# Kernel optimization log

Hardware: AMD Instinct MI355X
Metric: run time of the kernel (lower is better)

The kernel has to match this reference:

```python
import jax, jax.numpy as jnp
import numpy as np

N_NODES = 100000
N_EDGES = 3200000
F_IN = 128
F_OUT = 128


def setup_inputs() -> dict:
    key = jax.random.key(0)
    ks = jax.random.split(key, 6)
    stdv = 1.0 / np.sqrt(F_OUT)
    return {
        "x": jax.random.normal(ks[0], (N_NODES, F_IN), dtype=jnp.float32),
        "weight": jax.random.uniform(ks[1], (F_IN, F_OUT), minval=-stdv, maxval=stdv, dtype=jnp.float32),
        "bias": jax.random.uniform(ks[2], (F_OUT,), minval=-stdv, maxval=stdv, dtype=jnp.float32),
        "edge_src": jax.random.randint(ks[3], (N_EDGES,), 0, N_NODES, dtype=jnp.int32),
        "edge_dst": jax.random.randint(ks[4], (N_EDGES,), 0, N_NODES, dtype=jnp.int32),
        "edge_weight": jax.random.uniform(ks[5], (N_EDGES,), dtype=jnp.float32),
    }


def reference(x, weight, bias, edge_src, edge_dst, edge_weight):
    # Dense feature transform: support = X @ W  -> [N, F_OUT]
    support = jnp.matmul(x, weight)
    # Sparse adjacency aggregation (SpMM): out[d] = sum_e A[d, s_e] * support[s_e]
    msgs = support[edge_src] * edge_weight[:, None]  # [E, F_OUT]
    out = jax.ops.segment_sum(msgs, edge_dst, num_segments=N_NODES)
    return out + bias
```

## Files before the change

### kernel.cpp

```cpp
#include <hip/hip_runtime.h>

#define F 128
#define NB 64
#define MAXB 2048
#define NCHUNK 512
#define BCAP 3072

typedef __bf16 bf16x8 __attribute__((ext_vector_type(8)));
typedef unsigned short u16x8 __attribute__((ext_vector_type(8)));
typedef float f32x4 __attribute__((ext_vector_type(4)));

static __device__ __forceinline__ unsigned short f2bf(float f) {
    unsigned u = __float_as_uint(f);
    unsigned r = (u + 0x7FFF + ((u >> 16) & 1)) >> 16;
    return (unsigned short)r;
}

static __device__ __forceinline__ unsigned pack_rec(int src, int dl, float w) {
    unsigned wfix = (unsigned)(w * 511.0f + 0.5f);
    if (wfix > 511u) wfix = 511u;
    return (unsigned)src | ((unsigned)dl << 17) | (wfix << 23);
}

__global__ __launch_bounds__(256) void gemm_hist_kernel(const float* __restrict__ X,
                                                        const float* __restrict__ W,
                                                        unsigned short* __restrict__ Sb,
                                                        int n_nodes,
                                                        const int* __restrict__ edst,
                                                        int* __restrict__ counts,
                                                        int* __restrict__ bcnt,
                                                        int n_edges, int nbuck, int epc,
                                                        int ngemm) {
    __shared__ char smem[F * F * 2];
    int t = threadIdx.x;

    if ((int)blockIdx.x < ngemm) {
        unsigned short* WT = (unsigned short*)smem;
        {
            int f = t >> 1, half = t & 1;
#pragma unroll
            for (int j = 0; j < 8; ++j) {
                int k0 = half * 64 + j * 8;
                u16x8 pk;
#pragma unroll
                for (int i = 0; i < 8; ++i) pk[i] = f2bf(W[(size_t)(k0 + i) * F + f]);
                int byte = f * 256 + ((k0 * 2) ^ ((f & 7) << 4));
                *(u16x8*)((char*)WT + byte) = pk;
            }
        }
        __syncthreads();

        int w = t >> 6, l = t & 63;
        int lr = l & 15, lg = l >> 4;
        int rowBase = blockIdx.x * 128 + w * 32;

        f32x4 acc[2][8] = {};
        int r0 = rowBase + lr;
        int r1 = rowBase + 16 + lr;
        if (r0 >= n_nodes) r0 = n_nodes - 1;
        if (r1 >= n_nodes) r1 = n_nodes - 1;
        const float* a0p = X + (size_t)r0 * F + lg * 8;
        const float* a1p = X + (size_t)r1 * F + lg * 8;

#pragma unroll
        for (int kt = 0; kt < 4; ++kt) {
            float4 x0 = *(const float4*)(a0p + kt * 32);
            float4 x1 = *(const float4*)(a0p + kt * 32 + 4);
            u16x8 au;
            au[0] = f2bf(x0.x); au[1] = f2bf(x0.y); au[2] = f2bf(x0.z); au[3] = f2bf(x0.w);
            au[4] = f2bf(x1.x); au[5] = f2bf(x1.y); au[6] = f2bf(x1.z); au[7] = f2bf(x1.w);
            bf16x8 a0 = __builtin_bit_cast(bf16x8, au);
            float4 y0 = *(const float4*)(a1p + kt * 32);
            float4 y1 = *(const float4*)(a1p + kt * 32 + 4);
            au[0] = f2bf(y0.x); au[1] = f2bf(y0.y); au[2] = f2bf(y0.z); au[3] = f2bf(y0.w);
            au[4] = f2bf(y1.x); au[5] = f2bf(y1.y); au[6] = f2bf(y1.z); au[7] = f2bf(y1.w);
            bf16x8 a1 = __builtin_bit_cast(bf16x8, au);
#pragma unroll
            for (int ct = 0; ct < 8; ++ct) {
                int f = ct * 16 + lr;
                int byte = f * 256 + (((kt * 32 + lg * 8) * 2) ^ ((f & 7) << 4));
                bf16x8 bfr = *(bf16x8*)((char*)WT + byte);
                acc[0][ct] = __builtin_amdgcn_mfma_f32_16x16x32_bf16(a0, bfr, acc[0][ct], 0, 0, 0);
                acc[1][ct] = __builtin_amdgcn_mfma_f32_16x16x32_bf16(a1, bfr, acc[1][ct], 0, 0, 0);
            }
        }

#pragma unroll
        for (int tile = 0; tile < 2; ++tile) {
#pragma unroll
            for (int ct = 0; ct < 8; ++ct) {
                int col = ct * 16 + lr;
#pragma unroll
                for (int j = 0; j < 4; ++j) {
                    int row = rowBase + tile * 16 + lg * 4 + j;
                    if (row < n_nodes) Sb[(size_t)row * F + col] = f2bf(acc[tile][ct][j]);
                }
            }
        }
    } else {
        int* h = (int*)smem;
        int c = blockIdx.x - ngemm;
        for (int i = t; i < nbuck; i += 256) h[i] = 0;
        __syncthreads();
        int beg = c * epc, end = min(n_edges, beg + epc);
        for (int e0 = beg + t * 4; e0 < end; e0 += 1024) {
            if (e0 + 4 <= end) {
                int4 d4 = *(const int4*)&edst[e0];
                atomicAdd(&h[d4.x >> 6], 1);
                atomicAdd(&h[d4.y >> 6], 1);
                atomicAdd(&h[d4.z >> 6], 1);
                atomicAdd(&h[d4.w >> 6], 1);
            } else {
                for (int e = e0; e < end; ++e) atomicAdd(&h[edst[e] >> 6], 1);
            }
        }
        __syncthreads();
        for (int i = t; i < nbuck; i += 256) {
            int v = h[i];
            counts[(size_t)c * nbuck + i] = v;
            if (v) __hip_atomic_fetch_add(&bcnt[i], v, __ATOMIC_RELAXED, __HIP_MEMORY_SCOPE_AGENT);
        }
    }
}

__global__ __launch_bounds__(256) void bscan_kernel(const int* __restrict__ bcnt,
                                                    int* __restrict__ bstart, int nbuck) {
    __shared__ int tsum[256];
    int t = threadIdx.x;
    const int EPT = MAXB / 256;
    int base = t * EPT;
    int v[EPT];
    int s = 0;
#pragma unroll
    for (int i = 0; i < EPT; ++i) {
        int idx = base + i;
        v[i] = (idx < nbuck) ? bcnt[idx] : 0;
        s += v[i];
    }
    tsum[t] = s;
    __syncthreads();
    for (int off = 1; off < 256; off <<= 1) {
        int x = (t >= off) ? tsum[t - off] : 0;
        __syncthreads();
        tsum[t] += x;
        __syncthreads();
    }
    int run = tsum[t] - s;
#pragma unroll
    for (int i = 0; i < EPT; ++i) {
        int idx = base + i;
        if (idx < nbuck) {
            bstart[idx] = run;
            run += v[i];
        }
    }
    if (t == 255) bstart[nbuck] = run;
}

__global__ __launch_bounds__(256) void chunk_offs_kernel(const int* __restrict__ counts,
                                                         const int* __restrict__ bstart,
                                                         int* __restrict__ offs, int nbuck) {
    int wv = threadIdx.x >> 6, l = threadIdx.x & 63;
    int b = blockIdx.x * 4 + wv;
    if (b >= nbuck) return;
    const int CPL = NCHUNK / 64;
    int base = l * CPL;
    int v[CPL];
    int s = 0;
#pragma unroll
    for (int i = 0; i < CPL; ++i) {
        v[i] = counts[(size_t)(base + i) * nbuck + b];
        s += v[i];
    }
    int inc = s;
#pragma unroll
    for (int off = 1; off < 64; off <<= 1) {
        int up = __shfl_up(inc, off, 64);
        if (l >= off) inc += up;
    }
    int run = bstart[b] + inc - s;
#pragma unroll
    for (int i = 0; i < CPL; ++i) {
        offs[(size_t)(base + i) * nbuck + b] = run;
        run += v[i];
    }
}

__global__ __launch_bounds__(256) void chunk_scatter_kernel(const int* __restrict__ esrc,
                                                            const int* __restrict__ edst,
                                                            const float* __restrict__ ew,
                                                            const int* __restrict__ offs,
                                                            unsigned* __restrict__ ebuf,
                                                            int n_edges, int nbuck, int epc) {
    __shared__ int lcur[MAXB];
    int c = blockIdx.x, t = threadIdx.x;
    for (int i = t; i < nbuck; i += 256) lcur[i] = offs[(size_t)c * nbuck + i];
    __syncthreads();
    int beg = c * epc, end = min(n_edges, beg + epc);
    for (int e0 = beg + t * 4; e0 < end; e0 += 1024) {
        if (e0 + 4 <= end) {
            int4 s4 = *(const int4*)&esrc[e0];
            int4 d4 = *(const int4*)&edst[e0];
            float4 w4 = *(const float4*)&ew[e0];
            int pos;
            pos = atomicAdd(&lcur[d4.x >> 6], 1);
            ebuf[pos] = pack_rec(s4.x, d4.x & (NB - 1), w4.x);
            pos = atomicAdd(&lcur[d4.y >> 6], 1);
            ebuf[pos] = pack_rec(s4.y, d4.y & (NB - 1), w4.y);
            pos = atomicAdd(&lcur[d4.z >> 6], 1);
            ebuf[pos] = pack_rec(s4.z, d4.z & (NB - 1), w4.z);
            pos = atomicAdd(&lcur[d4.w >> 6], 1);
            ebuf[pos] = pack_rec(s4.w, d4.w & (NB - 1), w4.w);
        } else {
            for (int e = e0; e < end; ++e) {
                int d = edst[e];
                int pos = atomicAdd(&lcur[d >> 6], 1);
                ebuf[pos] = pack_rec(esrc[e], d & (NB - 1), ew[e]);
            }
        }
    }
}

__global__ __launch_bounds__(256) void local_sort_kernel(const unsigned* __restrict__ ebuf,
                                                         const int* __restrict__ bstart,
                                                         unsigned* __restrict__ csr,
                                                         int* __restrict__ rowst,
                                                         int* __restrict__ cnt_out, int n_nodes) {
    __shared__ int lcnt[NB];
    __shared__ int lcur[NB];
    __shared__ unsigned se[BCAP];
    int b = blockIdx.x, t = threadIdx.x;
    int beg = bstart[b], end = bstart[b + 1];
    int num = end - beg;
    bool inl = num <= BCAP;

    if (t < NB) lcnt[t] = 0;
    __syncthreads();

    for (int i = t; i < num; i += 256) {
        unsigned p = ebuf[beg + i];
        if (inl) se[i] = p;
        atomicAdd(&lcnt[(p >> 17) & (NB - 1)], 1);
    }
    __syncthreads();

    if (t < NB) {
        int v = lcnt[t];
        int inc = v;
#pragma unroll
        for (int off = 1; off < NB; off <<= 1) {
            int up = __shfl_up(inc, off, NB);
            if (t >= off) inc += up;
        }
        int excl = inc - v;
        lcur[t] = excl;
        int node = b * NB + t;
        if (node < n_nodes) {
            rowst[node] = beg + excl;
            cnt_out[node] = v;
        }
    }
    __syncthreads();

    for (int i = t; i < num; i += 256) {
        unsigned p = inl ? se[i] : ebuf[beg + i];
        int dl = (p >> 17) & (NB - 1);
        int pos = beg + atomicAdd(&lcur[dl], 1);
        csr[pos] = p;
    }
}

__global__ __launch_bounds__(256) void gather_kernel(const unsigned short* __restrict__ Sb,
                                                     const unsigned* __restrict__ csr,
                                                     const int* __restrict__ rowst,
                                                     const int* __restrict__ cnt,
                                                     const float* __restrict__ bias,
                                                     float* __restrict__ out, int n_nodes) {
    int node = blockIdx.x * 4 + (threadIdx.x >> 6);
    if (node >= n_nodes) return;
    int lane = threadIdx.x & 63;
    int half = lane >> 5, l32 = lane & 31;

    int beg = rowst[node];
    int num = cnt[node];
    int last = beg + num - 1;

    float4 acc = {0.f, 0.f, 0.f, 0.f};
    const unsigned short* sbp = Sb + l32 * 4;
    const float WSCALE = 1.0f / 511.0f;

    int i = 0;
    for (; i + 16 <= num; i += 16) {
        unsigned long long g[8];
        float wt[8];
#pragma unroll
        for (int j = 0; j < 8; ++j) {
            unsigned p = csr[beg + i + 2 * j + half];
            g[j] = *(const unsigned long long*)(sbp + (size_t)(p & 0x1FFFFu) * F);
            wt[j] = (float)(p >> 23) * WSCALE;
        }
#pragma unroll
        for (int j = 0; j < 8; ++j) {
            unsigned lo = (unsigned)g[j], hi = (unsigned)(g[j] >> 32);
            acc.x += wt[j] * __uint_as_float(lo << 16);
            acc.y += wt[j] * __uint_as_float(lo & 0xFFFF0000u);
            acc.z += wt[j] * __uint_as_float(hi << 16);
            acc.w += wt[j] * __uint_as_float(hi & 0xFFFF0000u);
        }
    }
    for (; i < num; i += 2) {
        bool live = (i + half) < num;
        unsigned p = csr[live ? beg + i + half : last];
        float wt = live ? (float)(p >> 23) * WSCALE : 0.f;
        unsigned long long g = *(const unsigned long long*)(sbp + (size_t)(p & 0x1FFFFu) * F);
        unsigned lo = (unsigned)g, hi = (unsigned)(g >> 32);
        acc.x += wt * __uint_as_float(lo << 16);
        acc.y += wt * __uint_as_float(lo & 0xFFFF0000u);
        acc.z += wt * __uint_as_float(hi << 16);
        acc.w += wt * __uint_as_float(hi & 0xFFFF0000u);
    }

    acc.x += __shfl_xor(acc.x, 32);
    acc.y += __shfl_xor(acc.y, 32);
    acc.z += __shfl_xor(acc.z, 32);
    acc.w += __shfl_xor(acc.w, 32);

    if (half == 0) {
        float4 bi = *(const float4*)&bias[l32 * 4];
        acc.x += bi.x; acc.y += bi.y; acc.z += bi.z; acc.w += bi.w;
        *(float4*)&out[(size_t)node * F + l32 * 4] = acc;
    }
}

__global__ __launch_bounds__(256) void init_out_kernel(float* __restrict__ out,
                                                       const float* __restrict__ bias,
                                                       int n_nodes) {
    int idx = blockIdx.x * blockDim.x + threadIdx.x;
    int total = n_nodes * F;
    if (idx < total) out[idx] = bias[idx & (F - 1)];
}

__global__ __launch_bounds__(256) void gemm_fb_kernel(const float* __restrict__ X,
                                                      const float* __restrict__ W,
                                                      unsigned short* __restrict__ Sb,
                                                      int n_nodes) {
    int idx = blockIdx.x * blockDim.x + threadIdx.x;
    int row = idx >> 5;
    int fb = (idx & 31) * 4;
    if (row >= n_nodes) return;
    const float* xr = X + (size_t)row * F;
    float a0 = 0, a1 = 0, a2 = 0, a3 = 0;
    for (int k = 0; k < F; ++k) {
        float xv = xr[k];
        const float* wr = W + (size_t)k * F + fb;
        a0 += xv * wr[0]; a1 += xv * wr[1]; a2 += xv * wr[2]; a3 += xv * wr[3];
    }
    ushort4 res;
    res.x = f2bf(a0); res.y = f2bf(a1); res.z = f2bf(a2); res.w = f2bf(a3);
    *(ushort4*)&Sb[(size_t)row * F + fb] = res;
}

__global__ __launch_bounds__(256) void scatter_edges_kernel(const unsigned short* __restrict__ Sb,
                                                            const int* __restrict__ esrc,
                                                            const int* __restrict__ edst,
                                                            const float* __restrict__ ew,
                                                            float* __restrict__ out,
                                                            int n_edges) {
    long long idx = (long long)blockIdx.x * blockDim.x + threadIdx.x;
    int e = (int)(idx >> 5);
    if (e >= n_edges) return;
    int fbase = ((int)idx & 31) * 4;
    int s = esrc[e];
    int d = edst[e];
    float w = ew[e];
    ushort4 v = *(const ushort4*)&Sb[(size_t)s * F + fbase];
    float* o = out + (size_t)d * F + fbase;
    __hip_atomic_fetch_add(&o[0], w * __uint_as_float((unsigned)v.x << 16), __ATOMIC_RELAXED, __HIP_MEMORY_SCOPE_AGENT);
    __hip_atomic_fetch_add(&o[1], w * __uint_as_float((unsigned)v.y << 16), __ATOMIC_RELAXED, __HIP_MEMORY_SCOPE_AGENT);
    __hip_atomic_fetch_add(&o[2], w * __uint_as_float((unsigned)v.z << 16), __ATOMIC_RELAXED, __HIP_MEMORY_SCOPE_AGENT);
    __hip_atomic_fetch_add(&o[3], w * __uint_as_float((unsigned)v.w << 16), __ATOMIC_RELAXED, __HIP_MEMORY_SCOPE_AGENT);
}

extern "C" void kernel_launch(void* const* d_in, const int* in_sizes, int n_in,
                              void* d_out, int out_size, void* d_ws, size_t ws_size,
                              hipStream_t stream) {
    const float* x    = (const float*)d_in[0];
    const float* w    = (const float*)d_in[1];
    const float* bias = (const float*)d_in[2];
    const int*   esrc = (const int*)d_in[3];
    const int*   edst = (const int*)d_in[4];
    const float* ew   = (const float*)d_in[5];
    float* out = (float*)d_out;

    int n_nodes = in_sizes[0] / F;
    int n_edges = in_sizes[3];
    int nbuck = (n_nodes + NB - 1) / NB;
    int epc = ((n_edges + NCHUNK - 1) / NCHUNK + 3) & ~3;

    size_t off = 0;
    auto carve = [&](size_t bytes) -> void* {
        void* p = (char*)d_ws + off;
        off += (bytes + 255) & ~(size_t)255;
        return p;
    };
    unsigned short* Sb    = (unsigned short*)carve((size_t)n_nodes * F * sizeof(unsigned short));
    unsigned*       ebuf  = (unsigned*)carve((size_t)n_edges * sizeof(unsigned));
    unsigned*       csr   = (unsigned*)carve((size_t)n_edges * sizeof(unsigned));
    int*            bcnt  = (int*)carve((size_t)nbuck * sizeof(int));
    int*            bst   = (int*)carve((size_t)(nbuck + 1) * sizeof(int));
    int*            rowst = (int*)carve((size_t)n_nodes * sizeof(int));
    int*            ncnt  = (int*)carve((size_t)n_nodes * sizeof(int));
    int*            counts = (int*)carve((size_t)NCHUNK * nbuck * sizeof(int));
    int*            offs   = (int*)carve((size_t)NCHUNK * nbuck * sizeof(int));
    bool ok = (off <= ws_size) && (nbuck <= MAXB) && (n_nodes <= (1 << 17));

    if (ok) {
        int ngemm = (n_nodes + 127) / 128;
        hipMemsetAsync(bcnt, 0, (size_t)nbuck * sizeof(int), stream);
        gemm_hist_kernel<<<ngemm + NCHUNK, 256, 0, stream>>>(x, w, Sb, n_nodes, edst, counts,
                                                             bcnt, n_edges, nbuck, epc, ngemm);
        bscan_kernel<<<1, 256, 0, stream>>>(bcnt, bst, nbuck);
        chunk_offs_kernel<<<(nbuck + 3) / 4, 256, 0, stream>>>(counts, bst, offs, nbuck);
        chunk_scatter_kernel<<<NCHUNK, 256, 0, stream>>>(esrc, edst, ew, offs, ebuf,
                                                         n_edges, nbuck, epc);
        local_sort_kernel<<<nbuck, 256, 0, stream>>>(ebuf, bst, csr, rowst, ncnt, n_nodes);
        gather_kernel<<<(n_nodes + 3) / 4, 256, 0, stream>>>(Sb, csr, rowst, ncnt, bias, out,
                                                             n_nodes);
    } else {
        gemm_fb_kernel<<<(n_nodes * 32 + 255) / 256, 256, 0, stream>>>(x, w, Sb, n_nodes);
        int total = n_nodes * F;
        init_out_kernel<<<(total + 255) / 256, 256, 0, stream>>>(out, bias, n_nodes);
        long long t2 = (long long)n_edges * 32;
        scatter_edges_kernel<<<(int)((t2 + 255) / 256), 256, 0, stream>>>(Sb, esrc, edst, ew, out,
                                                                          n_edges);
    }
}
```

Before: 222.4 us.

## Fuse per-bucket local sort with gather into one kernel using shared-memory CSR

Merges the local counting sort and the SpMM gather into a single kernel per 64-node bucket. The sorted edge records stay in LDS, and each of the 4 waves then aggregates 16 nodes from that buffer. This removes the global CSR write and re-read, the rowst/count arrays, and one kernel launch. In exchange the gather runs with only ~1563 blocks of 4 waves, each processing nodes serially, which reduces parallelism and latency hiding on the random Sb loads, and ebuf is now read twice.

```diff
diff --git a/kernel.cpp b/kernel.cpp
--- a/kernel.cpp
+++ b/kernel.cpp
@@ -221,14 +221,16 @@
     }
 }
 
-__global__ __launch_bounds__(256) void local_sort_kernel(const unsigned* __restrict__ ebuf,
-                                                         const int* __restrict__ bstart,
-                                                         unsigned* __restrict__ csr,
-                                                         int* __restrict__ rowst,
-                                                         int* __restrict__ cnt_out, int n_nodes) {
+__global__ __launch_bounds__(256) void sort_gather_kernel(const unsigned short* __restrict__ Sb,
+                                                          const unsigned* __restrict__ ebuf,
+                                                          const int* __restrict__ bstart,
+                                                          unsigned* __restrict__ csr,
+                                                          const float* __restrict__ bias,
+                                                          float* __restrict__ out, int n_nodes) {
+    __shared__ unsigned sorted[BCAP];
     __shared__ int lcnt[NB];
     __shared__ int lcur[NB];
-    __shared__ unsigned se[BCAP];
+    __shared__ int lrs[NB + 1];
     int b = blockIdx.x, t = threadIdx.x;
     int beg = bstart[b], end = bstart[b + 1];
     int num = end - beg;
@@ -238,9 +240,7 @@
     __syncthreads();
 
     for (int i = t; i < num; i += 256) {
-        unsigned p = ebuf[beg + i];
-        if (inl) se[i] = p;
-        atomicAdd(&lcnt[(p >> 17) & (NB - 1)], 1);
+        atomicAdd(&lcnt[(ebuf[beg + i] >> 17) & (NB - 1)], 1);
     }
     __syncthreads();
 
@@ -253,82 +253,77 @@
             if (t >= off) inc += up;
         }
         int excl = inc - v;
+        lrs[t] = excl;
         lcur[t] = excl;
-        int node = b * NB + t;
-        if (node < n_nodes) {
-            rowst[node] = beg + excl;
-            cnt_out[node] = v;
-        }
+        if (t == NB - 1) lrs[NB] = inc;
     }
     __syncthreads();
 
     for (int i = t; i < num; i += 256) {
-        unsigned p = inl ? se[i] : ebuf[beg + i];
-        int dl = (p >> 17) & (NB - 1);
-        int pos = beg + atomicAdd(&lcur[dl], 1);
-        csr[pos] = p;
-    }
-}
-
-__global__ __launch_bounds__(256) void gather_kernel(const unsigned short* __restrict__ Sb,
-                                                     const unsigned* __restrict__ csr,
-                                                     const int* __restrict__ rowst,
-                                                     const int* __restrict__ cnt,
-                                                     const float* __restrict__ bias,
-                                                     float* __restrict__ out, int n_nodes) {
-    int node = blockIdx.x * 4 + (threadIdx.x >> 6);
-    if (node >= n_nodes) return;
-    int lane = threadIdx.x & 63;
+        unsigned p = ebuf[beg + i];
+        int pos = atomicAdd(&lcur[(p >> 17) & (NB - 1)], 1);
+        if (inl) sorted[pos] = p;
+        else csr[beg + pos] = p;
+    }
+    __syncthreads();
+
+    int w = t >> 6, lane = t & 63;
     int half = lane >> 5, l32 = lane & 31;
-
-    int beg = rowst[node];
-    int num = cnt[node];
-    int last = beg + num - 1;
-
-    float4 acc = {0.f, 0.f, 0.f, 0.f};
     const unsigned short* sbp = Sb + l32 * 4;
     const float WSCALE = 1.0f / 511.0f;
 
-    int i = 0;
-    for (; i + 16 <= num; i += 16) {
-        unsigned long long g[8];
-        float wt[8];
-#pragma unroll
-        for (int j = 0; j < 8; ++j) {
-            unsigned p = csr[beg + i + 2 * j + half];
-            g[j] = *(const unsigned long long*)(sbp + (size_t)(p & 0x1FFFFu) * F);
-            wt[j] = (float)(p >> 23) * WSCALE;
-        }
-#pragma unroll
-        for (int j = 0; j < 8; ++j) {
-            unsigned lo = (unsigned)g[j], hi = (unsigned)(g[j] >> 32);
-            acc.x += wt[j] * __uint_as_float(lo << 16);
-            acc.y += wt[j] * __uint_as_float(lo & 0xFFFF0000u);
-            acc.z += wt[j] * __uint_as_float(hi << 16);
-            acc.w += wt[j] * __uint_as_float(hi & 0xFFFF0000u);
-        }
-    }
-    for (; i < num; i += 2) {
-        bool live = (i + half) < num;
-        unsigned p = csr[live ? beg + i + half : last];
-        float wt = live ? (float)(p >> 23) * WSCALE : 0.f;
-        unsigned long long g = *(const unsigned long long*)(sbp + (size_t)(p & 0x1FFFFu) * F);
-        unsigned lo = (unsigned)g, hi = (unsigned)(g >> 32);
-        acc.x += wt * __uint_as_float(lo << 16);
-        acc.y += wt * __uint_as_float(lo & 0xFFFF0000u);
-        acc.z += wt * __uint_as_float(hi << 16);
-        acc.w += wt * __uint_as_float(hi & 0xFFFF0000u);
-    }
-
-    acc.x += __shfl_xor(acc.x, 32);
-    acc.y += __shfl_xor(acc.y, 32);
-    acc.z += __shfl_xor(acc.z, 32);
-    acc.w += __shfl_xor(acc.w, 32);
-
-    if (half == 0) {
-        float4 bi = *(const float4*)&bias[l32 * 4];
-        acc.x += bi.x; acc.y += bi.y; acc.z += bi.z; acc.w += bi.w;
-        *(float4*)&out[(size_t)node * F + l32 * 4] = acc;
+    for (int k = 0; k < 16; ++k) {
+        int node_l = w * 16 + k;
+        int node = b * NB + node_l;
+        if (node >= n_nodes) break;
+        int s0 = lrs[node_l];
+        int cntn = lrs[node_l + 1] - s0;
+        int last = s0 + cntn - 1;
+
+        float4 acc = {0.f, 0.f, 0.f, 0.f};
+        int i = 0;
+        for (; i + 16 <= cntn; i += 16) {
+            unsigned long long g[8];
+            float wt[8];
+#pragma unroll
+            for (int j = 0; j < 8; ++j) {
+                int idx = s0 + i + 2 * j + half;
+                unsigned p = inl ? sorted[idx] : csr[beg + idx];
+                g[j] = *(const unsigned long long*)(sbp + (size_t)(p & 0x1FFFFu) * F);
+                wt[j] = (float)(p >> 23) * WSCALE;
+            }
+#pragma unroll
+            for (int j = 0; j < 8; ++j) {
+                unsigned lo = (unsigned)g[j], hi = (unsigned)(g[j] >> 32);
+                acc.x += wt[j] * __uint_as_float(lo << 16);
+                acc.y += wt[j] * __uint_as_float(lo & 0xFFFF0000u);
+                acc.z += wt[j] * __uint_as_float(hi << 16);
+                acc.w += wt[j] * __uint_as_float(hi & 0xFFFF0000u);
+            }
+        }
+        for (; i < cntn; i += 2) {
+            bool live = (i + half) < cntn;
+            int idx = live ? s0 + i + half : last;
+            unsigned p = inl ? sorted[idx] : csr[beg + idx];
+            float wt = live ? (float)(p >> 23) * WSCALE : 0.f;
+            unsigned long long g = *(const unsigned long long*)(sbp + (size_t)(p & 0x1FFFFu) * F);
+            unsigned lo = (unsigned)g, hi = (unsigned)(g >> 32);
+            acc.x += wt * __uint_as_float(lo << 16);
+            acc.y += wt * __uint_as_float(lo & 0xFFFF0000u);
+            acc.z += wt * __uint_as_float(hi << 16);
+            acc.w += wt * __uint_as_float(hi & 0xFFFF0000u);
+        }
+
+        acc.x += __shfl_xor(acc.x, 32);
+        acc.y += __shfl_xor(acc.y, 32);
+        acc.z += __shfl_xor(acc.z, 32);
+        acc.w += __shfl_xor(acc.w, 32);
+
+        if (half == 0) {
+            float4 bi = *(const float4*)&bias[l32 * 4];
+            acc.x += bi.x; acc.y += bi.y; acc.z += bi.z; acc.w += bi.w;
+            *(float4*)&out[(size_t)node * F + l32 * 4] = acc;
+        }
     }
 }
 
@@ -408,8 +403,6 @@
     unsigned*       csr   = (unsigned*)carve((size_t)n_edges * sizeof(unsigned));
     int*            bcnt  = (int*)carve((size_t)nbuck * sizeof(int));
     int*            bst   = (int*)carve((size_t)(nbuck + 1) * sizeof(int));
-    int*            rowst = (int*)carve((size_t)n_nodes * sizeof(int));
-    int*            ncnt  = (int*)carve((size_t)n_nodes * sizeof(int));
     int*            counts = (int*)carve((size_t)NCHUNK * nbuck * sizeof(int));
     int*            offs   = (int*)carve((size_t)NCHUNK * nbuck * sizeof(int));
     bool ok = (off <= ws_size) && (nbuck <= MAXB) && (n_nodes <= (1 << 17));
@@ -423,9 +416,7 @@
         chunk_offs_kernel<<<(nbuck + 3) / 4, 256, 0, stream>>>(counts, bst, offs, nbuck);
         chunk_scatter_kernel<<<NCHUNK, 256, 0, stream>>>(esrc, edst, ew, offs, ebuf,
                                                          n_edges, nbuck, epc);
-        local_sort_kernel<<<nbuck, 256, 0, stream>>>(ebuf, bst, csr, rowst, ncnt, n_nodes);
-        gather_kernel<<<(n_nodes + 3) / 4, 256, 0, stream>>>(Sb, csr, rowst, ncnt, bias, out,
-                                                             n_nodes);
+        sort_gather_kernel<<<nbuck, 256, 0, stream>>>(Sb, ebuf, bst, csr, bias, out, n_nodes);
     } else {
         gemm_fb_kernel<<<(n_nodes * 32 + 255) / 256, 256, 0, stream>>>(x, w, Sb, n_nodes);
         int total = n_nodes * F;
```

Measured after the change: 226.7 us. Within noise of the previous version (+1.9%).
